# Kernel optimization log

Hardware: AMD Instinct MI355X
Metric: run time of the kernel (lower is better)

The kernel has to match this reference:

```python
import jax, jax.numpy as jnp
import numpy as np
import math

B, T, C, H = 4, 2048, 1024, 16
D = C // H  # head dim = 64
W_STD = 0.02


def setup_inputs() -> dict:
    key = jax.random.key(0)
    kx, kw, kb = jax.random.split(key, 3)
    x = jax.random.normal(kx, (B, T, C), dtype=jnp.float32)
    # Linear params stored as [in, 3*in] for x @ W; scaled like typical init
    w_qkv = jax.random.normal(kw, (C, 3 * C), dtype=jnp.float32) * W_STD
    b_qkv = jax.random.normal(kb, (3 * C,), dtype=jnp.float32) * W_STD
    return {"x": x, "w_qkv": w_qkv, "b_qkv": b_qkv}


def reference(x, w_qkv, b_qkv):
    # Fused QKV projection; torch splits as keys, queries, values (in that order)
    qkv = x @ w_qkv + b_qkv                      # [B, T, 3C]
    k, q, v = jnp.split(qkv, 3, axis=-1)          # each [B, T, C]

    def heads(t):  # [B, T, C] -> [B, H, T, D]
        return t.reshape(B, T, H, D).transpose(0, 2, 1, 3)

    k, q, v = heads(k), heads(q), heads(v)
    scale = 1.0 / math.sqrt(D)
    logits = jnp.einsum("bhqd,bhkd->bhqk", q, k) * scale  # [B, H, T, T]
    causal = jnp.tril(jnp.ones((T, T), dtype=bool))
    logits = jnp.where(causal, logits, -jnp.inf)
    probs = jax.nn.softmax(logits, axis=-1)
    y = jnp.einsum("bhqk,bhkd->bhqd", probs, v)   # [B, H, T, D]
    return y.transpose(0, 2, 1, 3).reshape(B, T, C)
```

## Files before the change

kernel.cpp:

```cpp
#include <hip/hip_runtime.h>
#include <hip/hip_bf16.h>

typedef unsigned short ushort_t;
typedef __attribute__((ext_vector_type(4))) short bf16x4_t;
typedef __attribute__((ext_vector_type(8))) short short8;
typedef __attribute__((ext_vector_type(4))) unsigned short ushort4_t;
typedef __attribute__((ext_vector_type(4))) float f32x4;
typedef __attribute__((ext_vector_type(2))) unsigned int uint2_t;
typedef __attribute__((ext_vector_type(4))) unsigned int uint4_t;

#define LOG2E 1.44269504088896340736f

__device__ __forceinline__ unsigned short f2bf(float f) {
    unsigned int u = __float_as_uint(f);
    u += 0x7fffu + ((u >> 16) & 1u);
    return (unsigned short)(u >> 16);
}

__device__ __forceinline__ unsigned int pk2bf(float a, float b) {
    union { __hip_bfloat162 h2; unsigned int u; } cvt;
    cvt.h2 = __float22bfloat162_rn(make_float2(a, b));
    return cvt.u;
}

__device__ __forceinline__ void gl_lds16(const ushort_t* g, ushort_t* l) {
    __builtin_amdgcn_global_load_lds(
        (const __attribute__((address_space(1))) unsigned int*)g,
        (__attribute__((address_space(3))) unsigned int*)l, 16, 0, 0);
}

__device__ __forceinline__ f32x4 mfma16(uint2_t a, uint2_t b, f32x4 c) {
    union { uint2_t u; bf16x4_t s; } ua, ub;
    ua.u = a; ub.u = b;
    return __builtin_amdgcn_mfma_f32_16x16x16bf16_1k(ua.s, ub.s, c, 0, 0, 0);
}

__global__ __launch_bounds__(256) void cvt_xw(
    const float* __restrict__ x, ushort_t* __restrict__ xb,
    const float* __restrict__ w, ushort_t* __restrict__ wt)
{
    __shared__ ushort_t Ts[64][40];
    const int bid = blockIdx.x;
    const int tid = threadIdx.x;
    if (bid < 4096) {
        const size_t i = ((size_t)bid * 256 + tid) * 8;
        const float4 a = *(const float4*)(x + i);
        const float4 b = *(const float4*)(x + i + 4);
        uint4_t o;
        o[0] = pk2bf(a.x, a.y); o[1] = pk2bf(a.z, a.w);
        o[2] = pk2bf(b.x, b.y); o[3] = pk2bf(b.z, b.w);
        *(uint4_t*)(xb + i) = o;
    } else {
        const int wb = bid - 4096;
        const int k0 = (wb & 31) * 32, n0 = (wb >> 5) * 64;
        const int kr = tid >> 3, nc = (tid & 7) * 8;
        const float* g = w + (size_t)(k0 + kr) * 3072 + n0 + nc;
        const float4 a = *(const float4*)g;
        const float4 b = *(const float4*)(g + 4);
        const float vals[8] = {a.x, a.y, a.z, a.w, b.x, b.y, b.z, b.w};
#pragma unroll
        for (int j = 0; j < 8; ++j) Ts[nc + j][kr] = f2bf(vals[j]);
        __syncthreads();
        const int nr = tid >> 2, kc = (tid & 3) * 8;
        const short8 v = *(const short8*)&Ts[nr][kc];
        *(short8*)(wt + (size_t)(n0 + nr) * 1024 + k0 + kc) = v;
    }
}

__global__ __launch_bounds__(256) void qkv_gemm(
    const ushort_t* __restrict__ xb, const ushort_t* __restrict__ wt,
    const float* __restrict__ bq,
    ushort_t* __restrict__ kws, ushort_t* __restrict__ qws,
    ushort_t* __restrict__ vws)
{
    __shared__ ushort_t As[3][128 * 32];
    __shared__ ushort_t Bs[3][128 * 32];

    const int tid  = threadIdx.x;
    const int m0   = blockIdx.x * 128;
    const int n0   = blockIdx.y * 128;
    const int wv   = tid >> 6;
    const int lane = tid & 63;
    const int qr   = lane & 15;
    const int quad = lane >> 4;
    const int wm   = (wv >> 1) * 64;
    const int wn   = (wv & 1) * 64;

    const int lr   = lane >> 2;
    const int csw  = (lane & 3) ^ ((lr >> 1) & 3);
    const ushort_t* gA = xb + (size_t)(m0 + wv*32 + lr) * 1024 + csw*8;
    const ushort_t* gB = wt + (size_t)(n0 + wv*32 + lr) * 1024 + csw*8;
    const int sdst = wv * 1024;

    const int swq = quad ^ ((qr >> 1) & 3);

    f32x4 acc[4][4];
#pragma unroll
    for (int i = 0; i < 4; ++i)
#pragma unroll
        for (int j = 0; j < 4; ++j) acc[i][j] = (f32x4){0.f, 0.f, 0.f, 0.f};

    gl_lds16(gA,             (ushort_t*)As + sdst);
    gl_lds16(gA + 16*1024,   (ushort_t*)As + sdst + 512);
    gl_lds16(gB,             (ushort_t*)Bs + sdst);
    gl_lds16(gB + 16*1024,   (ushort_t*)Bs + sdst + 512);
    gl_lds16(gA + 32,            (ushort_t*)As + 4096 + sdst);
    gl_lds16(gA + 32 + 16*1024,  (ushort_t*)As + 4096 + sdst + 512);
    gl_lds16(gB + 32,            (ushort_t*)Bs + 4096 + sdst);
    gl_lds16(gB + 32 + 16*1024,  (ushort_t*)Bs + 4096 + sdst + 512);

    int bufc = 0;
    for (int kt = 0; kt < 32; ++kt) {
        if (kt < 31) asm volatile("s_waitcnt vmcnt(4)" ::: "memory");
        else         asm volatile("s_waitcnt vmcnt(0)" ::: "memory");
        __builtin_amdgcn_s_barrier();
        __builtin_amdgcn_sched_barrier(0);

        const ushort_t* cA = (const ushort_t*)As + bufc * 4096;
        const ushort_t* cB = (const ushort_t*)Bs + bufc * 4096;
        short8 af[4], bfr[4];
#pragma unroll
        for (int i = 0; i < 4; ++i)
            af[i] = *(const short8*)&cA[(wm + i*16 + qr) * 32 + swq * 8];
#pragma unroll
        for (int j = 0; j < 4; ++j)
            bfr[j] = *(const short8*)&cB[(wn + j*16 + qr) * 32 + swq * 8];

        if (kt < 30) {
            int b2 = bufc + 2;
            if (b2 >= 3) b2 -= 3;
            const int k2 = (kt + 2) * 32;
            ushort_t* dA = (ushort_t*)As + b2 * 4096 + sdst;
            ushort_t* dB = (ushort_t*)Bs + b2 * 4096 + sdst;
            gl_lds16(gA + k2,            dA);
            gl_lds16(gA + k2 + 16*1024,  dA + 512);
            gl_lds16(gB + k2,            dB);
            gl_lds16(gB + k2 + 16*1024,  dB + 512);
        }

#pragma unroll
        for (int i = 0; i < 4; ++i)
#pragma unroll
            for (int j = 0; j < 4; ++j)
                acc[i][j] = __builtin_amdgcn_mfma_f32_16x16x32_bf16(
                    af[i], bfr[j], acc[i][j], 0, 0, 0);

        asm volatile("s_waitcnt lgkmcnt(0)" ::: "memory");
        bufc = (bufc == 2) ? 0 : bufc + 1;
    }

    const int nbase = n0 + wn;
    const int sec   = nbase >> 10;
    const int h     = (nbase & 1023) >> 6;

    if (sec == 2) {
#pragma unroll
        for (int j = 0; j < 4; ++j) {
            const float bias = bq[nbase + j*16 + qr];
            const int d = j*16 + qr;
#pragma unroll
            for (int i = 0; i < 4; ++i) {
                const int m  = m0 + wm + i*16 + quad*4;
                const int bb = m >> 11;
                const int tt = m & 2047;
                ushort4_t pk;
#pragma unroll
                for (int r = 0; r < 4; ++r) pk[r] = f2bf(acc[i][j][r] + bias);
                *(ushort4_t*)&vws[((size_t)(bb*16 + h)*64 + d)*2048 + tt] = pk;
            }
        }
    } else {
        ushort_t* __restrict__ dst = (sec == 0) ? kws : qws;
#pragma unroll
        for (int j = 0; j < 4; ++j) {
            const float bias = bq[nbase + j*16 + qr];
            const int d = j*16 + qr;
#pragma unroll
            for (int i = 0; i < 4; ++i) {
#pragma unroll
                for (int r = 0; r < 4; ++r) {
                    const int m  = m0 + wm + i*16 + quad*4 + r;
                    const int bb = m >> 11;
                    const int tt = m & 2047;
                    dst[(((size_t)(bb*16 + h)) * 2048 + tt) * 64 + d] =
                        f2bf(acc[i][j][r] + bias);
                }
            }
        }
    }
}

__global__ __launch_bounds__(512) void attn_fwd(
    const ushort_t* __restrict__ kws, const ushort_t* __restrict__ qws,
    const ushort_t* __restrict__ vws, float* __restrict__ out)
{
    constexpr int LDK = 72;
    __shared__ ushort_t Ks[2][64 * LDK];
    __shared__ ushort_t Vs[2][64 * LDK];

    const int tid  = threadIdx.x;
    const int wv   = tid >> 6;
    const int lane = tid & 63;
    const int qr   = lane & 15;
    const int quad = lane >> 4;
    const int srow = tid >> 3;
    const int scol = (tid & 7) * 8;
    constexpr float SCL = 0.125f * LOG2E;
    constexpr float CB  = 8.0f;

    const int bid = (int)blockIdx.x;
    const int qt  = 15 - (bid >> 6);
    const int bh  = bid & 63;
    const size_t bhT = (size_t)bh * 2048;
    const ushort_t* kbase = kws + bhT * 64;
    const ushort_t* vbase = vws + (size_t)bh * 64 * 2048;
    const int b = bh >> 4, h = bh & 15;

    const int q0 = qt * 128;
    const int base = q0 + wv*16;
    const int qv0 = base + qr;

    const ushort_t* qg0 = qws + (bhT + qv0) * 64;
    const short8 Qb00 = *(const short8*)(qg0 + quad*8);
    const short8 Qb01 = *(const short8*)(qg0 + 32 + quad*8);

    float l_s = 0.f;
    f32x4 Oacc[4];
#pragma unroll
    for (int dt = 0; dt < 4; ++dt) Oacc[dt] = (f32x4){0.f,0.f,0.f,0.f};

    const int nkt = 2*qt + 2;
    const int row_max = base + 15;

    short8 kv0, vv0;
    {
        const ushort_t* kg = kbase + (size_t)srow * 64 + scol;
        const ushort_t* vg = vbase + (size_t)srow * 2048 + scol;
        kv0 = *(const short8*)(kg);
        vv0 = *(const short8*)(vg);
    }
    *(short8*)&Ks[0][srow * LDK + scol] = kv0;
    *(short8*)&Vs[0][srow * LDK + scol] = vv0;
    __syncthreads();

    for (int kt = 0; kt < nkt; ++kt) {
        const int k0 = kt * 64;
        const int cur = kt & 1;
        const bool more = (kt + 1 < nkt);
        if (more) {
            const ushort_t* kg = kbase + (size_t)(k0 + 64 + srow) * 64 + scol;
            const ushort_t* vg = vbase + (size_t)srow * 2048 + k0 + 64 + scol;
            kv0 = *(const short8*)(kg);
            vv0 = *(const short8*)(vg);
        }

        if (k0 <= row_max) {
            const ushort_t* Kc = Ks[cur];
            const ushort_t* Vc = Vs[cur];
            const bool diag = (k0 + 63 > base);

            uint2_t pks[4];
            float ps0 = 0.f;
#pragma unroll
            for (int t4 = 0; t4 < 4; ++t4) {
                const short8 kf0 = *(const short8*)&Kc[(t4*16 + qr)*LDK + quad*8];
                const short8 kf1 = *(const short8*)&Kc[(t4*16 + qr)*LDK + 32 + quad*8];
                f32x4 a = (f32x4){0.f,0.f,0.f,0.f};
                a = __builtin_amdgcn_mfma_f32_16x16x32_bf16(kf0, Qb00, a, 0,0,0);
                a = __builtin_amdgcn_mfma_f32_16x16x32_bf16(kf1, Qb01, a, 0,0,0);
                if (diag) {
#pragma unroll
                    for (int r = 0; r < 4; ++r) {
                        const int key = k0 + t4*16 + quad*4 + r;
                        if (key > qv0) a[r] = -INFINITY;
                    }
                }
                float p0[4];
#pragma unroll
                for (int r = 0; r < 4; ++r) {
                    p0[r] = exp2f(__builtin_fmaf(a[r], SCL, -CB));
                    ps0 += p0[r];
                }
                pks[t4][0] = pk2bf(p0[0], p0[1]);
                pks[t4][1] = pk2bf(p0[2], p0[3]);
            }
            l_s += ps0;

            __builtin_amdgcn_s_setprio(1);
#pragma unroll
            for (int dt = 0; dt < 4; ++dt) {
#pragma unroll
                for (int t4 = 0; t4 < 4; ++t4) {
                    const uint2_t vf = *(const uint2_t*)
                        &Vc[(dt*16 + qr)*LDK + t4*16 + quad*4];
                    Oacc[dt] = mfma16(pks[t4], vf, Oacc[dt]);
                }
            }
            __builtin_amdgcn_s_setprio(0);
        }

        if (more) {
            *(short8*)&Ks[cur ^ 1][srow * LDK + scol] = kv0;
            *(short8*)&Vs[cur ^ 1][srow * LDK + scol] = vv0;
        }
        __syncthreads();
    }

    float lf = l_s;
    lf += __shfl_xor(lf, 16);
    lf += __shfl_xor(lf, 32);
#pragma unroll
    for (int r = 0; r < 4; ++r) {
        const float lr  = __shfl(lf, quad*4 + r);
        const float inv = 1.f / lr;
        const int q = q0 + wv*16 + quad*4 + r;
        float* o = out + ((size_t)(b*2048 + q)) * 1024 + h*64;
#pragma unroll
        for (int dt = 0; dt < 4; ++dt) o[dt*16 + qr] = Oacc[dt][r] * inv;
    }
}

extern "C" void kernel_launch(void* const* d_in, const int* in_sizes, int n_in,
                              void* d_out, int out_size, void* d_ws, size_t ws_size,
                              hipStream_t stream) {
    (void)in_sizes; (void)n_in; (void)out_size; (void)ws_size;
    const float* x  = (const float*)d_in[0];
    const float* w  = (const float*)d_in[1];
    const float* bq = (const float*)d_in[2];
    float* out = (float*)d_out;

    ushort_t* kws = (ushort_t*)d_ws;
    ushort_t* qws = kws + (size_t)8388608;
    ushort_t* vws = qws + (size_t)8388608;
    ushort_t* xb  = vws + (size_t)8388608;
    ushort_t* wt  = xb  + (size_t)8388608;

    cvt_xw<<<5632, 256, 0, stream>>>(x, xb, w, wt);
    qkv_gemm<<<dim3(64, 24), 256, 0, stream>>>(xb, wt, bq, kws, qws, vws);
    attn_fwd<<<1024, 512, 0, stream>>>(kws, qws, vws, out);
}
```

Before: 216.3 us.

## Split attention KV range across two wave groups and merge partial outputs in LDS

The 8 waves become two groups of 4. Each group processes half of the causal KV tiles for the same 128-query block, and each wave now handles 32 query rows so every K/V fragment read from LDS feeds twice as many MFMAs. Group 1 writes its unnormalized partial O and row sums into LDS, and group 0 adds them in before normalizing. This cuts the serial KV loop length and raises reuse of LDS reads. The cost is double the shared memory, more registers per wave, and a final LDS reduction step.

```diff
diff --git a/kernel.cpp b/kernel.cpp
--- a/kernel.cpp
+++ b/kernel.cpp
@@ -195,16 +195,19 @@
     const ushort_t* __restrict__ vws, float* __restrict__ out)
 {
     constexpr int LDK = 72;
-    __shared__ ushort_t Ks[2][64 * LDK];
-    __shared__ ushort_t Vs[2][64 * LDK];
+    constexpr int LSO = 68;
+    __shared__ ushort_t smem[2][2][2][64 * LDK];
 
     const int tid  = threadIdx.x;
     const int wv   = tid >> 6;
+    const int g    = wv >> 2;
+    const int gw   = wv & 3;
     const int lane = tid & 63;
     const int qr   = lane & 15;
     const int quad = lane >> 4;
-    const int srow = tid >> 3;
-    const int scol = (tid & 7) * 8;
+    const int t256 = tid & 255;
+    const int srow = t256 >> 2;
+    const int scol = (t256 & 3) * 16;
     constexpr float SCL = 0.125f * LOG2E;
     constexpr float CB  = 8.0f;
 
@@ -214,77 +217,94 @@
     const size_t bhT = (size_t)bh * 2048;
     const ushort_t* kbase = kws + bhT * 64;
     const ushort_t* vbase = vws + (size_t)bh * 64 * 2048;
-    const int b = bh >> 4, h = bh & 15;
-
-    const int q0 = qt * 128;
-    const int base = q0 + wv*16;
-    const int qv0 = base + qr;
+    const int b = bh >> 4, hh = bh & 15;
+
+    const int hf    = qt + 1;
+    const int tile0 = g * hf;
+    const int q0    = qt * 128;
+    const int base  = q0 + gw * 32;
+    const int qv0   = base + qr;
+    const int qv1   = qv0 + 16;
+    const int row_max = base + 31;
 
     const ushort_t* qg0 = qws + (bhT + qv0) * 64;
+    const ushort_t* qg1 = qws + (bhT + qv1) * 64;
     const short8 Qb00 = *(const short8*)(qg0 + quad*8);
     const short8 Qb01 = *(const short8*)(qg0 + 32 + quad*8);
-
-    float l_s = 0.f;
-    f32x4 Oacc[4];
-#pragma unroll
-    for (int dt = 0; dt < 4; ++dt) Oacc[dt] = (f32x4){0.f,0.f,0.f,0.f};
-
-    const int nkt = 2*qt + 2;
-    const int row_max = base + 15;
-
-    short8 kv0, vv0;
+    const short8 Qb10 = *(const short8*)(qg1 + quad*8);
+    const short8 Qb11 = *(const short8*)(qg1 + 32 + quad*8);
+
+    float l_s[2] = {0.f, 0.f};
+    f32x4 Oacc[2][4];
+#pragma unroll
+    for (int qs = 0; qs < 2; ++qs)
+#pragma unroll
+        for (int dt = 0; dt < 4; ++dt) Oacc[qs][dt] = (f32x4){0.f,0.f,0.f,0.f};
+
+    short8 kv0, kv1, vv0, vv1;
     {
-        const ushort_t* kg = kbase + (size_t)srow * 64 + scol;
-        const ushort_t* vg = vbase + (size_t)srow * 2048 + scol;
-        kv0 = *(const short8*)(kg);
-        vv0 = *(const short8*)(vg);
-    }
-    *(short8*)&Ks[0][srow * LDK + scol] = kv0;
-    *(short8*)&Vs[0][srow * LDK + scol] = vv0;
+        const ushort_t* kg = kbase + (size_t)(tile0*64 + srow) * 64 + scol;
+        const ushort_t* vg = vbase + (size_t)srow * 2048 + tile0*64 + scol;
+        kv0 = *(const short8*)(kg);     kv1 = *(const short8*)(kg + 8);
+        vv0 = *(const short8*)(vg);     vv1 = *(const short8*)(vg + 8);
+    }
+    *(short8*)&smem[g][0][0][srow * LDK + scol]     = kv0;
+    *(short8*)&smem[g][0][0][srow * LDK + scol + 8] = kv1;
+    *(short8*)&smem[g][1][0][srow * LDK + scol]     = vv0;
+    *(short8*)&smem[g][1][0][srow * LDK + scol + 8] = vv1;
     __syncthreads();
 
-    for (int kt = 0; kt < nkt; ++kt) {
-        const int k0 = kt * 64;
-        const int cur = kt & 1;
-        const bool more = (kt + 1 < nkt);
+    for (int it = 0; it < hf; ++it) {
+        const int k0  = (tile0 + it) * 64;
+        const int cur = it & 1;
+        const bool more = (it + 1 < hf);
         if (more) {
             const ushort_t* kg = kbase + (size_t)(k0 + 64 + srow) * 64 + scol;
             const ushort_t* vg = vbase + (size_t)srow * 2048 + k0 + 64 + scol;
-            kv0 = *(const short8*)(kg);
-            vv0 = *(const short8*)(vg);
+            kv0 = *(const short8*)(kg);   kv1 = *(const short8*)(kg + 8);
+            vv0 = *(const short8*)(vg);   vv1 = *(const short8*)(vg + 8);
         }
 
         if (k0 <= row_max) {
-            const ushort_t* Kc = Ks[cur];
-            const ushort_t* Vc = Vs[cur];
+            const ushort_t* Kc = smem[g][0][cur];
+            const ushort_t* Vc = smem[g][1][cur];
             const bool diag = (k0 + 63 > base);
 
-            uint2_t pks[4];
-            float ps0 = 0.f;
+            uint2_t pks[2][4];
+            float ps0 = 0.f, ps1 = 0.f;
 #pragma unroll
             for (int t4 = 0; t4 < 4; ++t4) {
                 const short8 kf0 = *(const short8*)&Kc[(t4*16 + qr)*LDK + quad*8];
                 const short8 kf1 = *(const short8*)&Kc[(t4*16 + qr)*LDK + 32 + quad*8];
                 f32x4 a = (f32x4){0.f,0.f,0.f,0.f};
-                a = __builtin_amdgcn_mfma_f32_16x16x32_bf16(kf0, Qb00, a, 0,0,0);
-                a = __builtin_amdgcn_mfma_f32_16x16x32_bf16(kf1, Qb01, a, 0,0,0);
+                f32x4 bfr = (f32x4){0.f,0.f,0.f,0.f};
+                a   = __builtin_amdgcn_mfma_f32_16x16x32_bf16(kf0, Qb00, a, 0,0,0);
+                a   = __builtin_amdgcn_mfma_f32_16x16x32_bf16(kf1, Qb01, a, 0,0,0);
+                bfr = __builtin_amdgcn_mfma_f32_16x16x32_bf16(kf0, Qb10, bfr, 0,0,0);
+                bfr = __builtin_amdgcn_mfma_f32_16x16x32_bf16(kf1, Qb11, bfr, 0,0,0);
                 if (diag) {
 #pragma unroll
                     for (int r = 0; r < 4; ++r) {
                         const int key = k0 + t4*16 + quad*4 + r;
-                        if (key > qv0) a[r] = -INFINITY;
+                        if (key > qv0) a[r]   = -INFINITY;
+                        if (key > qv1) bfr[r] = -INFINITY;
                     }
                 }
-                float p0[4];
+                float p0[4], p1[4];
 #pragma unroll
                 for (int r = 0; r < 4; ++r) {
-                    p0[r] = exp2f(__builtin_fmaf(a[r], SCL, -CB));
+                    p0[r] = exp2f(__builtin_fmaf(a[r],   SCL, -CB));
+                    p1[r] = exp2f(__builtin_fmaf(bfr[r], SCL, -CB));
                     ps0 += p0[r];
+                    ps1 += p1[r];
                 }
-                pks[t4][0] = pk2bf(p0[0], p0[1]);
-                pks[t4][1] = pk2bf(p0[2], p0[3]);
-            }
-            l_s += ps0;
+                pks[0][t4][0] = pk2bf(p0[0], p0[1]);
+                pks[0][t4][1] = pk2bf(p0[2], p0[3]);
+                pks[1][t4][0] = pk2bf(p1[0], p1[1]);
+                pks[1][t4][1] = pk2bf(p1[2], p1[3]);
+            }
+            l_s[0] += ps0;
+            l_s[1] += ps1;
 
             __builtin_amdgcn_s_setprio(1);
 #pragma unroll
@@ -293,30 +313,62 @@
                 for (int t4 = 0; t4 < 4; ++t4) {
                     const uint2_t vf = *(const uint2_t*)
                         &Vc[(dt*16 + qr)*LDK + t4*16 + quad*4];
-                    Oacc[dt] = mfma16(pks[t4], vf, Oacc[dt]);
+                    Oacc[0][dt] = mfma16(pks[0][t4], vf, Oacc[0][dt]);
+                    Oacc[1][dt] = mfma16(pks[1][t4], vf, Oacc[1][dt]);
                 }
             }
             __builtin_amdgcn_s_setprio(0);
         }
 
         if (more) {
-            *(short8*)&Ks[cur ^ 1][srow * LDK + scol] = kv0;
-            *(short8*)&Vs[cur ^ 1][srow * LDK + scol] = vv0;
+            *(short8*)&smem[g][0][cur^1][srow * LDK + scol]     = kv0;
+            *(short8*)&smem[g][0][cur^1][srow * LDK + scol + 8] = kv1;
+            *(short8*)&smem[g][1][cur^1][srow * LDK + scol]     = vv0;
+            *(short8*)&smem[g][1][cur^1][srow * LDK + scol + 8] = vv1;
         }
         __syncthreads();
     }
 
-    float lf = l_s;
-    lf += __shfl_xor(lf, 16);
-    lf += __shfl_xor(lf, 32);
-#pragma unroll
-    for (int r = 0; r < 4; ++r) {
-        const float lr  = __shfl(lf, quad*4 + r);
-        const float inv = 1.f / lr;
-        const int q = q0 + wv*16 + quad*4 + r;
-        float* o = out + ((size_t)(b*2048 + q)) * 1024 + h*64;
-#pragma unroll
-        for (int dt = 0; dt < 4; ++dt) o[dt*16 + qr] = Oacc[dt][r] * inv;
+    float lf[2];
+#pragma unroll
+    for (int qs = 0; qs < 2; ++qs) {
+        float v = l_s[qs];
+        v += __shfl_xor(v, 16);
+        v += __shfl_xor(v, 32);
+        lf[qs] = v;
+    }
+
+    float* Ls = (float*)smem;
+    if (g == 1) {
+#pragma unroll
+        for (int qs = 0; qs < 2; ++qs) {
+#pragma unroll
+            for (int dt = 0; dt < 4; ++dt)
+#pragma unroll
+                for (int r = 0; r < 4; ++r)
+                    Ls[(gw*32 + qs*16 + quad*4 + r)*LSO + dt*16 + qr]
+                        = Oacc[qs][dt][r];
+            if (quad == 0)
+                Ls[(gw*32 + qs*16 + qr)*LSO + 64] = lf[qs];
+        }
+    }
+    __syncthreads();
+    if (g == 0) {
+#pragma unroll
+        for (int qs = 0; qs < 2; ++qs) {
+#pragma unroll
+            for (int r = 0; r < 4; ++r) {
+                const int ql  = gw*32 + qs*16 + quad*4 + r;
+                const float lr  = __shfl(lf[qs], quad*4 + r) + Ls[ql*LSO + 64];
+                const float inv = 1.f / lr;
+                const int q = q0 + ql;
+                float* o = out + ((size_t)(b*2048 + q)) * 1024 + hh*64;
+#pragma unroll
+                for (int dt = 0; dt < 4; ++dt)
+                    o[dt*16 + qr] = (Oacc[qs][dt][r]
+                                     + Ls[ql*LSO + dt*16 + qr]) * inv;
+            }
+        }
     }
 }
 
```

Result: slower. 245.2 us (+13.4%).

## Give each attention wave two 16-row query tiles, halving waves per block

Applied to the files above, without the earlier changes.

The attention kernel now runs 4 waves per 128-query block instead of 8, and each wave handles 32 query rows as two 16-row sub-tiles. Each K and V fragment read from LDS is reused for two sets of MFMAs, which halves LDS fragment traffic per FLOP. Each thread now stages 16 elements of K and V per tile instead of 8. The cost is more registers per wave and fewer waves to hide latency. The diagonal tile also does more masked work per wave, because the causal check now covers 32 rows.

```diff
diff --git a/kernel.cpp b/kernel.cpp
--- a/kernel.cpp
+++ b/kernel.cpp
@@ -190,7 +190,7 @@
     }
 }
 
-__global__ __launch_bounds__(512) void attn_fwd(
+__global__ __launch_bounds__(256) void attn_fwd(
     const ushort_t* __restrict__ kws, const ushort_t* __restrict__ qws,
     const ushort_t* __restrict__ vws, float* __restrict__ out)
 {
@@ -203,8 +203,8 @@
     const int lane = tid & 63;
     const int qr   = lane & 15;
     const int quad = lane >> 4;
-    const int srow = tid >> 3;
-    const int scol = (tid & 7) * 8;
+    const int srow = tid >> 2;
+    const int scol = (tid & 3) * 16;
     constexpr float SCL = 0.125f * LOG2E;
     constexpr float CB  = 8.0f;
 
@@ -216,31 +216,39 @@
     const ushort_t* vbase = vws + (size_t)bh * 64 * 2048;
     const int b = bh >> 4, h = bh & 15;
 
-    const int q0 = qt * 128;
-    const int base = q0 + wv*16;
-    const int qv0 = base + qr;
+    const int q0   = qt * 128;
+    const int base = q0 + wv*32;
+    const int qv0  = base + qr;
+    const int qv1  = qv0 + 16;
 
     const ushort_t* qg0 = qws + (bhT + qv0) * 64;
+    const ushort_t* qg1 = qws + (bhT + qv1) * 64;
     const short8 Qb00 = *(const short8*)(qg0 + quad*8);
     const short8 Qb01 = *(const short8*)(qg0 + 32 + quad*8);
-
-    float l_s = 0.f;
-    f32x4 Oacc[4];
-#pragma unroll
-    for (int dt = 0; dt < 4; ++dt) Oacc[dt] = (f32x4){0.f,0.f,0.f,0.f};
+    const short8 Qb10 = *(const short8*)(qg1 + quad*8);
+    const short8 Qb11 = *(const short8*)(qg1 + 32 + quad*8);
+
+    float l_s[2] = {0.f, 0.f};
+    f32x4 Oacc[2][4];
+#pragma unroll
+    for (int qs = 0; qs < 2; ++qs)
+#pragma unroll
+        for (int dt = 0; dt < 4; ++dt) Oacc[qs][dt] = (f32x4){0.f,0.f,0.f,0.f};
 
     const int nkt = 2*qt + 2;
-    const int row_max = base + 15;
-
-    short8 kv0, vv0;
+    const int row_max = base + 31;
+
+    short8 kv0, kv1, vv0, vv1;
     {
         const ushort_t* kg = kbase + (size_t)srow * 64 + scol;
         const ushort_t* vg = vbase + (size_t)srow * 2048 + scol;
-        kv0 = *(const short8*)(kg);
-        vv0 = *(const short8*)(vg);
-    }
-    *(short8*)&Ks[0][srow * LDK + scol] = kv0;
-    *(short8*)&Vs[0][srow * LDK + scol] = vv0;
+        kv0 = *(const short8*)(kg);     kv1 = *(const short8*)(kg + 8);
+        vv0 = *(const short8*)(vg);     vv1 = *(const short8*)(vg + 8);
+    }
+    *(short8*)&Ks[0][srow * LDK + scol]     = kv0;
+    *(short8*)&Ks[0][srow * LDK + scol + 8] = kv1;
+    *(short8*)&Vs[0][srow * LDK + scol]     = vv0;
+    *(short8*)&Vs[0][srow * LDK + scol + 8] = vv1;
     __syncthreads();
 
     for (int kt = 0; kt < nkt; ++kt) {
@@ -250,8 +258,8 @@
         if (more) {
             const ushort_t* kg = kbase + (size_t)(k0 + 64 + srow) * 64 + scol;
             const ushort_t* vg = vbase + (size_t)srow * 2048 + k0 + 64 + scol;
-            kv0 = *(const short8*)(kg);
-            vv0 = *(const short8*)(vg);
+            kv0 = *(const short8*)(kg);   kv1 = *(const short8*)(kg + 8);
+            vv0 = *(const short8*)(vg);   vv1 = *(const short8*)(vg + 8);
         }
 
         if (k0 <= row_max) {
@@ -259,32 +267,41 @@
             const ushort_t* Vc = Vs[cur];
             const bool diag = (k0 + 63 > base);
 
-            uint2_t pks[4];
-            float ps0 = 0.f;
+            uint2_t pks[2][4];
+            float ps0 = 0.f, ps1 = 0.f;
 #pragma unroll
             for (int t4 = 0; t4 < 4; ++t4) {
                 const short8 kf0 = *(const short8*)&Kc[(t4*16 + qr)*LDK + quad*8];
                 const short8 kf1 = *(const short8*)&Kc[(t4*16 + qr)*LDK + 32 + quad*8];
                 f32x4 a = (f32x4){0.f,0.f,0.f,0.f};
-                a = __builtin_amdgcn_mfma_f32_16x16x32_bf16(kf0, Qb00, a, 0,0,0);
-                a = __builtin_amdgcn_mfma_f32_16x16x32_bf16(kf1, Qb01, a, 0,0,0);
+                f32x4 bfr = (f32x4){0.f,0.f,0.f,0.f};
+                a   = __builtin_amdgcn_mfma_f32_16x16x32_bf16(kf0, Qb00, a, 0,0,0);
+                a   = __builtin_amdgcn_mfma_f32_16x16x32_bf16(kf1, Qb01, a, 0,0,0);
+                bfr = __builtin_amdgcn_mfma_f32_16x16x32_bf16(kf0, Qb10, bfr, 0,0,0);
+                bfr = __builtin_amdgcn_mfma_f32_16x16x32_bf16(kf1, Qb11, bfr, 0,0,0);
                 if (diag) {
 #pragma unroll
                     for (int r = 0; r < 4; ++r) {
                         const int key = k0 + t4*16 + quad*4 + r;
-                        if (key > qv0) a[r] = -INFINITY;
+                        if (key > qv0) a[r]   = -INFINITY;
+                        if (key > qv1) bfr[r] = -INFINITY;
                     }
                 }
-                float p0[4];
+                float p0[4], p1[4];
 #pragma unroll
                 for (int r = 0; r < 4; ++r) {
-                    p0[r] = exp2f(__builtin_fmaf(a[r], SCL, -CB));
+                    p0[r] = exp2f(__builtin_fmaf(a[r],   SCL, -CB));
+                    p1[r] = exp2f(__builtin_fmaf(bfr[r], SCL, -CB));
                     ps0 += p0[r];
+                    ps1 += p1[r];
                 }
-                pks[t4][0] = pk2bf(p0[0], p0[1]);
-                pks[t4][1] = pk2bf(p0[2], p0[3]);
+                pks[0][t4][0] = pk2bf(p0[0], p0[1]);
+                pks[0][t4][1] = pk2bf(p0[2], p0[3]);
+                pks[1][t4][0] = pk2bf(p1[0], p1[1]);
+                pks[1][t4][1] = pk2bf(p1[2], p1[3]);
             }
-            l_s += ps0;
+            l_s[0] += ps0;
+            l_s[1] += ps1;
 
             __builtin_amdgcn_s_setprio(1);
 #pragma unroll
@@ -293,30 +310,36 @@
                 for (int t4 = 0; t4 < 4; ++t4) {
                     const uint2_t vf = *(const uint2_t*)
                         &Vc[(dt*16 + qr)*LDK + t4*16 + quad*4];
-                    Oacc[dt] = mfma16(pks[t4], vf, Oacc[dt]);
+                    Oacc[0][dt] = mfma16(pks[0][t4], vf, Oacc[0][dt]);
+                    Oacc[1][dt] = mfma16(pks[1][t4], vf, Oacc[1][dt]);
                 }
             }
             __builtin_amdgcn_s_setprio(0);
         }
 
         if (more) {
-            *(short8*)&Ks[cur ^ 1][srow * LDK + scol] = kv0;
-            *(short8*)&Vs[cur ^ 1][srow * LDK + scol] = vv0;
+            *(short8*)&Ks[cur ^ 1][srow * LDK + scol]     = kv0;
+            *(short8*)&Ks[cur ^ 1][srow * LDK + scol + 8] = kv1;
+            *(short8*)&Vs[cur ^ 1][srow * LDK + scol]     = vv0;
+            *(short8*)&Vs[cur ^ 1][srow * LDK + scol + 8] = vv1;
         }
         __syncthreads();
     }
 
-    float lf = l_s;
-    lf += __shfl_xor(lf, 16);
-    lf += __shfl_xor(lf, 32);
-#pragma unroll
-    for (int r = 0; r < 4; ++r) {
-        const float lr  = __shfl(lf, quad*4 + r);
-        const float inv = 1.f / lr;
-        const int q = q0 + wv*16 + quad*4 + r;
-        float* o = out + ((size_t)(b*2048 + q)) * 1024 + h*64;
-#pragma unroll
-        for (int dt = 0; dt < 4; ++dt) o[dt*16 + qr] = Oacc[dt][r] * inv;
+#pragma unroll
+    for (int qs = 0; qs < 2; ++qs) {
+        float lf = l_s[qs];
+        lf += __shfl_xor(lf, 16);
+        lf += __shfl_xor(lf, 32);
+#pragma unroll
+        for (int r = 0; r < 4; ++r) {
+            const float lr  = __shfl(lf, quad*4 + r);
+            const float inv = 1.f / lr;
+            const int q = q0 + wv*32 + qs*16 + quad*4 + r;
+            float* o = out + ((size_t)(b*2048 + q)) * 1024 + h*64;
+#pragma unroll
+            for (int dt = 0; dt < 4; ++dt) o[dt*16 + qr] = Oacc[qs][dt][r] * inv;
+        }
     }
 }
 
@@ -337,5 +360,5 @@
 
     cvt_xw<<<5632, 256, 0, stream>>>(x, xb, w, wt);
     qkv_gemm<<<dim3(64, 24), 256, 0, stream>>>(xb, wt, bq, kws, qws, vws);
-    attn_fwd<<<1024, 512, 0, stream>>>(kws, qws, vws, out);
-}
+    attn_fwd<<<1024, 256, 0, stream>>>(kws, qws, vws, out);
+}
```

Result: slower. 225.4 us (+4.2%).

## Split long causal attention rows across two blocks and combine partials

Applied to the files above, without the earlier changes.

Query tiles in the upper half of the sequence are now processed by two blocks, each covering half of the key range. Their partial outputs and row sums are merged by a new combine kernel, and a lookup table orders the work items so the grid stays balanced. This shortens the longest per-block critical path of the causal attention and gives more blocks for the GPU's compute units. The cost is an extra kernel launch plus extra global writes and reads for the partial sums. A fixed exponent offset is kept instead of a running max, so merging partials only needs the two sums. The old kernel remains as a fallback when the workspace is too small.

```diff
diff --git a/kernel.cpp b/kernel.cpp
--- a/kernel.cpp
+++ b/kernel.cpp
@@ -34,6 +34,11 @@
     ua.u = a; ub.u = b;
     return __builtin_amdgcn_mfma_f32_16x16x16bf16_1k(ua.s, ub.s, c, 0, 0, 0);
 }
+
+__device__ const signed char QT_TAB[24] =
+    {15,15,7,14,14,13,13,6,12,12,11,11,5,10,10,9,9,4,8,8,3,2,1,0};
+__device__ const signed char GR_TAB[24] =
+    { 0, 1,2, 0, 1, 0, 1,2, 0, 1, 0, 1,2, 0, 1,0,1,2,0,1,2,2,2,2};
 
 __global__ __launch_bounds__(256) void cvt_xw(
     const float* __restrict__ x, ushort_t* __restrict__ xb,
@@ -190,9 +195,11 @@
     }
 }
 
-__global__ __launch_bounds__(512) void attn_fwd(
+
+__global__ __launch_bounds__(512) void attn_fwd_split(
     const ushort_t* __restrict__ kws, const ushort_t* __restrict__ qws,
-    const ushort_t* __restrict__ vws, float* __restrict__ out)
+    const ushort_t* __restrict__ vws, float* __restrict__ out,
+    float* __restrict__ pO1, float* __restrict__ pL)
 {
     constexpr int LDK = 72;
     __shared__ ushort_t Ks[2][64 * LDK];
@@ -208,6 +215,192 @@
     constexpr float SCL = 0.125f * LOG2E;
     constexpr float CB  = 8.0f;
 
+    const int bid  = (int)blockIdx.x;
+    const int item = bid >> 6;
+    const int bh   = bid & 63;
+    const int qt   = QT_TAB[item];
+    const int gr   = GR_TAB[item];
+    const size_t bhT = (size_t)bh * 2048;
+    const ushort_t* kbase = kws + bhT * 64;
+    const ushort_t* vbase = vws + (size_t)bh * 64 * 2048;
+    const int b = bh >> 4, h = bh & 15;
+
+    const int nt    = (gr == 2) ? (2*qt + 2) : (qt + 1);
+    const int tile0 = (gr == 1) ? (qt + 1) : 0;
+    const int q0    = qt * 128;
+    const int base  = q0 + wv*16;
+    const int qv0   = base + qr;
+    const int row_max = base + 15;
+
+    const ushort_t* qg0 = qws + (bhT + qv0) * 64;
+    const short8 Qb00 = *(const short8*)(qg0 + quad*8);
+    const short8 Qb01 = *(const short8*)(qg0 + 32 + quad*8);
+
+    float l_s = 0.f;
+    f32x4 Oacc[4];
+#pragma unroll
+    for (int dt = 0; dt < 4; ++dt) Oacc[dt] = (f32x4){0.f,0.f,0.f,0.f};
+
+    short8 kv0, vv0;
+    {
+        const ushort_t* kg = kbase + (size_t)(tile0*64 + srow) * 64 + scol;
+        const ushort_t* vg = vbase + (size_t)srow * 2048 + tile0*64 + scol;
+        kv0 = *(const short8*)(kg);
+        vv0 = *(const short8*)(vg);
+    }
+    *(short8*)&Ks[0][srow * LDK + scol] = kv0;
+    *(short8*)&Vs[0][srow * LDK + scol] = vv0;
+    __syncthreads();
+
+    for (int t = 0; t < nt; ++t) {
+        const int k0  = (tile0 + t) * 64;
+        const int cur = t & 1;
+        const bool more = (t + 1 < nt);
+        if (more) {
+            const ushort_t* kg = kbase + (size_t)(k0 + 64 + srow) * 64 + scol;
+            const ushort_t* vg = vbase + (size_t)srow * 2048 + k0 + 64 + scol;
+            kv0 = *(const short8*)(kg);
+            vv0 = *(const short8*)(vg);
+        }
+
+        if (k0 <= row_max) {
+            const ushort_t* Kc = Ks[cur];
+            const ushort_t* Vc = Vs[cur];
+            const bool diag = (k0 + 63 > base);
+
+            uint2_t pks[4];
+            float ps0 = 0.f;
+#pragma unroll
+            for (int t4 = 0; t4 < 4; ++t4) {
+                const short8 kf0 = *(const short8*)&Kc[(t4*16 + qr)*LDK + quad*8];
+                const short8 kf1 = *(const short8*)&Kc[(t4*16 + qr)*LDK + 32 + quad*8];
+                f32x4 a = (f32x4){0.f,0.f,0.f,0.f};
+                a = __builtin_amdgcn_mfma_f32_16x16x32_bf16(kf0, Qb00, a, 0,0,0);
+                a = __builtin_amdgcn_mfma_f32_16x16x32_bf16(kf1, Qb01, a, 0,0,0);
+                if (diag) {
+#pragma unroll
+                    for (int r = 0; r < 4; ++r) {
+                        const int key = k0 + t4*16 + quad*4 + r;
+                        if (key > qv0) a[r] = -INFINITY;
+                    }
+                }
+                float p0[4];
+#pragma unroll
+                for (int r = 0; r < 4; ++r) {
+                    p0[r] = exp2f(__builtin_fmaf(a[r], SCL, -CB));
+                    ps0 += p0[r];
+                }
+                pks[t4][0] = pk2bf(p0[0], p0[1]);
+                pks[t4][1] = pk2bf(p0[2], p0[3]);
+            }
+            l_s += ps0;
+
+            __builtin_amdgcn_s_setprio(1);
+#pragma unroll
+            for (int dt = 0; dt < 4; ++dt) {
+#pragma unroll
+                for (int t4 = 0; t4 < 4; ++t4) {
+                    const uint2_t vf = *(const uint2_t*)
+                        &Vc[(dt*16 + qr)*LDK + t4*16 + quad*4];
+                    Oacc[dt] = mfma16(pks[t4], vf, Oacc[dt]);
+                }
+            }
+            __builtin_amdgcn_s_setprio(0);
+        }
+
+        if (more) {
+            *(short8*)&Ks[cur ^ 1][srow * LDK + scol] = kv0;
+            *(short8*)&Vs[cur ^ 1][srow * LDK + scol] = vv0;
+        }
+        __syncthreads();
+    }
+
+    float lf = l_s;
+    lf += __shfl_xor(lf, 16);
+    lf += __shfl_xor(lf, 32);
+
+    if (gr == 2) {
+#pragma unroll
+        for (int r = 0; r < 4; ++r) {
+            const float lr  = __shfl(lf, quad*4 + r);
+            const float inv = 1.f / lr;
+            const int q = q0 + wv*16 + quad*4 + r;
+            float* o = out + ((size_t)(b*2048 + q)) * 1024 + h*64;
+#pragma unroll
+            for (int dt = 0; dt < 4; ++dt) o[dt*16 + qr] = Oacc[dt][r] * inv;
+        }
+    } else {
+        const int qtidx = qt - 8;
+        if (quad == 0)
+            pL[((size_t)(gr*64 + bh)*8 + qtidx)*128 + wv*16 + qr] = lf;
+        if (gr == 0) {
+#pragma unroll
+            for (int r = 0; r < 4; ++r) {
+                const int q = q0 + wv*16 + quad*4 + r;
+                float* o = out + ((size_t)(b*2048 + q)) * 1024 + h*64;
+#pragma unroll
+                for (int dt = 0; dt < 4; ++dt) o[dt*16 + qr] = Oacc[dt][r];
+            }
+        } else {
+#pragma unroll
+            for (int r = 0; r < 4; ++r) {
+                const int ql = wv*16 + quad*4 + r;
+                float* p = pO1 + (((size_t)bh*8 + qtidx)*128 + ql)*64;
+#pragma unroll
+                for (int dt = 0; dt < 4; ++dt) p[dt*16 + qr] = Oacc[dt][r];
+            }
+        }
+    }
+}
+
+__global__ __launch_bounds__(256) void attn_combine(
+    float* __restrict__ out, const float* __restrict__ pO1,
+    const float* __restrict__ pL)
+{
+    const int bid   = (int)blockIdx.x;
+    const int bh    = bid & 63;
+    const int qtidx = bid >> 6;
+    const int b = bh >> 4, h = bh & 15;
+    const int q0 = (8 + qtidx) * 128;
+
+    const int tid = threadIdx.x;
+    const int row = tid >> 1;
+    const int d0  = (tid & 1) * 32;
+
+    const size_t li = ((size_t)bh*8 + qtidx)*128 + row;
+    const float l0 = pL[li];
+    const float l1 = pL[(size_t)64*8*128 + li];
+    const float inv = 1.f / (l0 + l1);
+
+    float4* ov = (float4*)(out + ((size_t)(b*2048 + q0 + row))*1024 + h*64 + d0);
+    const float4* pv = (const float4*)(pO1 + (((size_t)bh*8 + qtidx)*128 + row)*64 + d0);
+#pragma unroll
+    for (int j = 0; j < 8; ++j) {
+        const float4 a = ov[j];
+        const float4 c = pv[j];
+        ov[j] = make_float4((a.x + c.x)*inv, (a.y + c.y)*inv,
+                            (a.z + c.z)*inv, (a.w + c.w)*inv);
+    }
+}
+
+__global__ __launch_bounds__(512) void attn_fwd(
+    const ushort_t* __restrict__ kws, const ushort_t* __restrict__ qws,
+    const ushort_t* __restrict__ vws, float* __restrict__ out)
+{
+    constexpr int LDK = 72;
+    __shared__ ushort_t Ks[2][64 * LDK];
+    __shared__ ushort_t Vs[2][64 * LDK];
+
+    const int tid  = threadIdx.x;
+    const int wv   = tid >> 6;
+    const int lane = tid & 63;
+    const int qr   = lane & 15;
+    const int quad = lane >> 4;
+    const int srow = tid >> 3;
+    const int scol = (tid & 7) * 8;
+    constexpr float SCL = 0.125f * LOG2E;
+    constexpr float CB  = 8.0f;
+
     const int bid = (int)blockIdx.x;
     const int qt  = 15 - (bid >> 6);
     const int bh  = bid & 63;
@@ -323,7 +516,7 @@
 extern "C" void kernel_launch(void* const* d_in, const int* in_sizes, int n_in,
                               void* d_out, int out_size, void* d_ws, size_t ws_size,
                               hipStream_t stream) {
-    (void)in_sizes; (void)n_in; (void)out_size; (void)ws_size;
+    (void)in_sizes; (void)n_in; (void)out_size;
     const float* x  = (const float*)d_in[0];
     const float* w  = (const float*)d_in[1];
     const float* bq = (const float*)d_in[2];
@@ -335,7 +528,18 @@
     ushort_t* xb  = vws + (size_t)8388608;
     ushort_t* wt  = xb  + (size_t)8388608;
 
+    float* pO1 = (float*)(wt + (size_t)8388608);
+    float* pL  = pO1 + (size_t)64*8*128*64;
+    const size_t ws_need = (size_t)5*16777216
+                         + (size_t)64*8*128*64*4
+                         + (size_t)2*64*8*128*4;
+
     cvt_xw<<<5632, 256, 0, stream>>>(x, xb, w, wt);
     qkv_gemm<<<dim3(64, 24), 256, 0, stream>>>(xb, wt, bq, kws, qws, vws);
-    attn_fwd<<<1024, 512, 0, stream>>>(kws, qws, vws, out);
-}
+    if (ws_size >= ws_need) {
+        attn_fwd_split<<<1536, 512, 0, stream>>>(kws, qws, vws, out, pO1, pL);
+        attn_combine<<<512, 256, 0, stream>>>(out, pO1, pL);
+    } else {
+        attn_fwd<<<1024, 512, 0, stream>>>(kws, qws, vws, out);
+    }
+}
```

After: 236.8 us. 9.4% more time.
